# Kernel optimization log

Hardware: AMD Instinct MI355X
Metric: run time of the kernel (lower is better)

The kernel has to match this reference:

```python
import jax, jax.numpy as jnp
import numpy as np

N_NODES = 50000
N_EDGES = 600000
D_IN = 128
D_OUT = 128
N_BASES = 4
N_RATINGS = 5


def setup_inputs() -> dict:
    key = jax.random.key(0)
    k1, k2, k3, k4, k5, k6 = jax.random.split(key, 6)
    x = jax.random.normal(k1, (N_NODES, D_IN), dtype=jnp.float32)
    edge_index = jax.random.randint(k2, (2, N_EDGES), 0, N_NODES, dtype=jnp.int64)
    edge_type = jax.random.randint(k3, (N_EDGES,), 0, N_RATINGS, dtype=jnp.int64)
    # basis matrices B_k: (out, in); a_r stacked over ratings: (R, K); W_0: (out, in)
    B = jax.random.normal(k4, (N_BASES, D_OUT, D_IN), dtype=jnp.float32) * 0.05
    A = jax.random.normal(k5, (N_RATINGS, N_BASES), dtype=jnp.float32) * 0.05
    W0 = jax.random.normal(k6, (D_OUT, D_IN), dtype=jnp.float32) * 0.05
    return {"x": x, "edge_index": edge_index, "edge_type": edge_type, "B": B, "A": A, "W0": W0}


def reference(x, edge_index, edge_type, B, A, W0):
    # self-loop term: (W0 @ x^T)^T == x @ W0^T
    n_nodes = x.shape[0]
    src, tgt = edge_index[0], edge_index[1]
    out = x @ W0.T  # [N, out]
    # per-relation basis-composed weights W_r = sum_k a_r[k] * B_k  -> [R, out, in]
    W = jnp.einsum('rk,kod->rod', A, B)
    n_ratings = A.shape[0]
    for r in range(n_ratings):  # small fixed relation set
        h = x @ W[r].T                     # [N, out] transform once per node
        msg = jnp.where((edge_type == r)[:, None], h[src], jnp.float32(0))  # [E, out]
        out = out + jax.ops.segment_sum(msg, tgt, num_segments=n_nodes)
    return out
```

## Files before the change

kernel.cpp:

```cpp
#include <hip/hip_runtime.h>

#define N_NODES 50000
#define N_EDGES 600000
#define D 128
#define NB_SCAN 196

typedef __attribute__((ext_vector_type(8))) short short8;
typedef __attribute__((ext_vector_type(4))) float float4v;

static __device__ __forceinline__ float bf2f(unsigned int u16) {
    union { unsigned int i; float f; } v; v.i = u16 << 16; return v.f;
}
static __device__ __forceinline__ unsigned short f2bf(float f) {
    union { float f; unsigned int i; } v; v.f = f;
    unsigned int u = v.i;
    return (unsigned short)((u + 0x7FFFu + ((u >> 16) & 1u)) >> 16);
}
static __device__ __forceinline__ float h2f(unsigned int h) {
    unsigned int s = (h >> 15) & 1u, e = (h >> 10) & 0x1fu, m = h & 0x3ffu;
    unsigned int bits = (e == 0) ? (s << 31)
                                 : ((s << 31) | ((e + 112u) << 23) | (m << 13));
    union { unsigned int i; float f; } v; v.i = bits; return v.f;
}

__global__ __launch_bounds__(256) void setup(int* __restrict__ flags,
                                             int* __restrict__ cnt,
                                             unsigned int* __restrict__ scanst) {
    int i = blockIdx.x * 256 + threadIdx.x;
    if (i < N_NODES) cnt[i] = 0;
    if (i < 8) flags[i] = 0;
    if (i < 200) scanst[i] = 0;
}

__global__ __launch_bounds__(256) void detect_all(const int* __restrict__ ei,
                                                  const int* __restrict__ et,
                                                  const unsigned int* __restrict__ x,
                                                  const unsigned int* __restrict__ B,
                                                  const unsigned int* __restrict__ A,
                                                  const unsigned int* __restrict__ W0,
                                                  int* __restrict__ flags) {
    __shared__ int sflag;
    if (threadIdx.x == 0) sflag = 0;
    __syncthreads();
    int b = blockIdx.x, acc = 0, fidx;
    if (b < 192) {
        fidx = 0;
        for (int i = b * 256 + threadIdx.x; i < N_EDGES; i += 192 * 256)
            acc |= ei[2 * i + 1];
    } else if (b < 240) {
        fidx = 1;
        for (int i = (b - 192) * 256 + threadIdx.x; i < N_EDGES / 2; i += 48 * 256)
            acc |= et[2 * i + 1];
    } else if (b < 288) {
        fidx = 2;
        for (int i = (b - 240) * 256 + threadIdx.x; i < 600000; i += 48 * 256) {
            unsigned int e = (x[i] >> 7) & 0xffu;
            acc |= (e > 0xA0u || e < 0x50u) ? 1 : 0;
        }
    } else if (b < 300) {
        fidx = 3;
        for (int i = (b - 288) * 256 + threadIdx.x; i < 32768; i += 12 * 256) {
            unsigned int e = (B[i] >> 7) & 0xffu;
            acc |= (e > 0xA0u || e < 0x50u) ? 1 : 0;
        }
    } else if (b == 300) {
        fidx = 4;
        for (int i = threadIdx.x; i < 10; i += 256) {
            unsigned int e = (A[i] >> 7) & 0xffu;
            acc |= (e > 0xA0u || e < 0x50u) ? 1 : 0;
        }
    } else if (b < 307) {
        fidx = 5;
        for (int i = (b - 301) * 256 + threadIdx.x; i < 8192; i += 6 * 256) {
            unsigned int e = (W0[i] >> 7) & 0xffu;
            acc |= (e > 0xA0u || e < 0x50u) ? 1 : 0;
        }
    } else {
        fidx = 6;
        for (int i = (b - 307) * 256 + threadIdx.x; i < 300000; i += 48 * 256) {
            unsigned int el = (x[i] >> 7) & 0xffu, eh = (x[i] >> 23) & 0xffu;
            acc |= (el < 0x58u || eh < 0x58u) ? 1 : 0;
        }
    }
    if (acc) sflag = 1;
    __syncthreads();
    if (threadIdx.x == 0 && sflag) atomicOr(flags + fidx, 1);
}

static __device__ __forceinline__ float loadw(const void* p, int idx, int f32) {
    return f32 ? ((const float*)p)[idx] : bf2f(((const unsigned short*)p)[idx]);
}

__global__ __launch_bounds__(256) void norm_hist_w(const int* __restrict__ ei,
                                                   const int* __restrict__ et,
                                                   int* __restrict__ idx32,
                                                   int* __restrict__ et32,
                                                   int* __restrict__ cnt,
                                                   const void* __restrict__ A,
                                                   const void* __restrict__ B,
                                                   const void* __restrict__ W0,
                                                   unsigned short* __restrict__ wcatW,
                                                   const int* __restrict__ flags) {
    int b = blockIdx.x;
    if (b < 4688) {
        int i = b * 256 + threadIdx.x;
        if (i < 2 * N_EDGES) {
            int v = flags[0] ? ei[i] : ei[2 * i];
            idx32[i] = v;
            if (i >= N_EDGES && (unsigned)v < (unsigned)N_NODES)
                atomicAdd(&cnt[v], 1);
        }
    } else if (b < 7032) {
        int i = (b - 4688) * 256 + threadIdx.x;
        if (i < N_EDGES) et32[i] = flags[1] ? et[i] : et[2 * i];
    } else {
        int idx = (b - 7032) * 256 + threadIdx.x;
        int fB = flags[3], fA = flags[4], fW = flags[5];
        int f = idx >> 7, d = idx & 127;
        int slot = f >> 7, o = f & 127;
        float v;
        if (slot == 0) {
            v = loadw(W0, o * D + d, fW);
        } else {
            int r = slot - 1;
            v = 0.f;
#pragma unroll
            for (int j = 0; j < 4; ++j)
                v += loadw(A, r * 4 + j, fA) * loadw(B, (j * D + o) * D + d, fB);
        }
        wcatW[idx] = f2bf(v);
    }
}

__global__ __launch_bounds__(256) void prep_wt6_direct(const void* __restrict__ A,
                                                       const void* __restrict__ B,
                                                       const void* __restrict__ W0,
                                                       float* __restrict__ wcatT6F,
                                                       const int* __restrict__ flags) {
    int idx = blockIdx.x * 256 + threadIdx.x;
    int fB = flags[3], fA = flags[4], fW = flags[5];
    int slot = idx >> 14, d = (idx >> 7) & 127, o = idx & 127;
    float v;
    if (slot == 0) {
        v = loadw(W0, o * D + d, fW);
    } else {
        int r = slot - 1;
        v = 0.f;
#pragma unroll
        for (int j = 0; j < 4; ++j)
            v += loadw(A, r * 4 + j, fA) * loadw(B, (j * D + o) * D + d, fB);
    }
    wcatT6F[idx] = v;
}

__global__ __launch_bounds__(256) void gemm_y(const void* __restrict__ xraw,
                                              const unsigned short* __restrict__ wcatW,
                                              unsigned short* __restrict__ Ybf,
                                              const int* __restrict__ flags) {
    __shared__ unsigned short xs[64 * 136];
    __shared__ unsigned short wsd[128 * 136];
    int tid = threadIdx.x;
    int m0 = blockIdx.x * 64;
    int wid = tid >> 6, lane = tid & 63;
    int wm = (wid & 1) * 32, wn = (wid >> 1) * 64;
    int lm = lane & 15, kg = lane >> 4;
    int f32 = flags[2], f16 = flags[6];
    const short8 z8 = {0, 0, 0, 0, 0, 0, 0, 0};

    {
        int row = tid >> 2, cseg = (tid & 3) * 32;
        int gm = m0 + row;
        short8 av[4];
        if (gm >= N_NODES) {
#pragma unroll
            for (int q = 0; q < 4; ++q) av[q] = z8;
        } else if (f32) {
            const float4* xp = (const float4*)xraw + (((size_t)gm * D + cseg) >> 2);
#pragma unroll
            for (int q = 0; q < 4; ++q) {
                float4 u0 = xp[2 * q], u1 = xp[2 * q + 1];
                union { short8 s; unsigned short h[8]; } pk;
                pk.h[0] = f2bf(u0.x); pk.h[1] = f2bf(u0.y);
                pk.h[2] = f2bf(u0.z); pk.h[3] = f2bf(u0.w);
                pk.h[4] = f2bf(u1.x); pk.h[5] = f2bf(u1.y);
                pk.h[6] = f2bf(u1.z); pk.h[7] = f2bf(u1.w);
                av[q] = pk.s;
            }
        } else if (f16) {
            const uint4* xp4 = (const uint4*)xraw + (((size_t)gm * D + cseg) >> 3);
#pragma unroll
            for (int q = 0; q < 4; ++q) {
                uint4 u = xp4[q];
                unsigned int ww[4] = {u.x, u.y, u.z, u.w};
                union { short8 s; unsigned short h[8]; } pk;
#pragma unroll
                for (int z = 0; z < 4; ++z) {
                    pk.h[2 * z]     = f2bf(h2f(ww[z] & 0xffffu));
                    pk.h[2 * z + 1] = f2bf(h2f(ww[z] >> 16));
                }
                av[q] = pk.s;
            }
        } else {
            const uint4* xp4 = (const uint4*)xraw + (((size_t)gm * D + cseg) >> 3);
#pragma unroll
            for (int q = 0; q < 4; ++q) {
                union { uint4 v; short8 s; } cv; cv.v = xp4[q];
                av[q] = cv.s;
            }
        }
#pragma unroll
        for (int q = 0; q < 4; ++q)
            *(short8*)(&xs[row * 136 + cseg + q * 8]) = av[q];
    }

    for (int nt = 0; nt < 6; ++nt) {
        if (nt) __syncthreads();
        {
            int row = tid >> 1, cseg = (tid & 1) * 64;
            const unsigned short* wp = wcatW + (size_t)(nt * 128 + row) * D + cseg;
#pragma unroll
            for (int q = 0; q < 8; ++q)
                *(short8*)(&wsd[row * 136 + cseg + q * 8]) = *(const short8*)(wp + q * 8);
        }
        __syncthreads();

        float4v accf[2][4];
#pragma unroll
        for (int i = 0; i < 2; ++i)
#pragma unroll
            for (int j = 0; j < 4; ++j) accf[i][j] = (float4v){0.f, 0.f, 0.f, 0.f};

#pragma unroll
        for (int kb = 0; kb < 4; ++kb) {
            int k = kb * 32 + kg * 8;
            short8 a[2], b[4];
#pragma unroll
            for (int i = 0; i < 2; ++i)
                a[i] = *(const short8*)(&xs[(wm + i * 16 + lm) * 136 + k]);
#pragma unroll
            for (int j = 0; j < 4; ++j)
                b[j] = *(const short8*)(&wsd[(wn + j * 16 + lm) * 136 + k]);
#pragma unroll
            for (int i = 0; i < 2; ++i)
#pragma unroll
                for (int j = 0; j < 4; ++j)
                    accf[i][j] = __builtin_amdgcn_mfma_f32_16x16x32_bf16(a[i], b[j], accf[i][j], 0, 0, 0);
        }

#pragma unroll
        for (int i = 0; i < 2; ++i) {
            int gmb = m0 + wm + i * 16 + kg * 4;
#pragma unroll
            for (int j = 0; j < 4; ++j) {
                int gn = nt * 128 + wn + j * 16 + lm;
#pragma unroll
                for (int r = 0; r < 4; ++r) {
                    int gm = gmb + r;
                    if (gm < N_NODES) Ybf[(size_t)gm * 768 + gn] = f2bf(accf[i][j][r]);
                }
            }
        }
    }
}

#define SC_AGG (1u << 30)
#define SC_PRE (1u << 31)
__global__ __launch_bounds__(256) void scan_place(const int* __restrict__ cnt,
                                                  int* __restrict__ offsets,
                                                  int* __restrict__ cursor,
                                                  unsigned int* __restrict__ scanst,
                                                  const int* __restrict__ src,
                                                  const int* __restrict__ tgt,
                                                  const int* __restrict__ et,
                                                  int* __restrict__ entries) {
    __shared__ int sh[256];
    __shared__ int sbid, sprefix;
    unsigned int* status = scanst;
    unsigned int* ticket = scanst + 196;
    unsigned int* done   = scanst + 197;
    int t = threadIdx.x;
    if (t == 0) sbid = (int)atomicAdd(ticket, 1u);
    __syncthreads();
    int bid = sbid;
    int idx = bid * 256 + t;
    int v = (idx < N_NODES) ? cnt[idx] : 0;
    sh[t] = v;
    __syncthreads();
    for (int off = 1; off < 256; off <<= 1) {
        int a = (t >= off) ? sh[t - off] : 0;
        __syncthreads();
        sh[t] += a;
        __syncthreads();
    }
    if (t == 0) {
        int total = sh[255];
        atomicExch(&status[bid], (unsigned int)total | SC_AGG);
        int prefix = 0;
        for (int j = bid - 1; j >= 0; --j) {
            unsigned int s;
            do { s = atomicAdd(&status[j], 0u); } while ((s & (SC_AGG | SC_PRE)) == 0u);
            prefix += (int)(s & 0x3FFFFFFFu);
            if (s & SC_PRE) break;
        }
        atomicExch(&status[bid], (unsigned int)(prefix + total) | SC_PRE);
        sprefix = prefix;
    }
    __syncthreads();
    int excl = sh[t] - v + sprefix;
    if (idx < N_NODES) {
        offsets[idx] = excl;
        atomicExch(&cursor[idx], excl);
        if (idx == N_NODES - 1) offsets[N_NODES] = excl + v;
    }
    __syncthreads();
    if (t == 0) {
        atomicAdd(done, 1u);
        while (atomicAdd(done, 0u) < (unsigned)NB_SCAN) __builtin_amdgcn_s_sleep(1);
    }
    __syncthreads();
    int e0 = bid * 3062;
    int e1 = e0 + 3062; if (e1 > N_EDGES) e1 = N_EDGES;
    for (int e = e0 + t; e < e1; e += 256) {
        int s = src[e], g = tgt[e], r = et[e];
        if ((unsigned)s >= (unsigned)N_NODES || (unsigned)g >= (unsigned)N_NODES || (unsigned)r >= 5u) continue;
        int pos = atomicAdd(&cursor[g], 1);
        entries[pos] = s * 8 + r;
    }
}

__global__ __launch_bounds__(256) void agg_out(const int* __restrict__ offsets,
                                               const int* __restrict__ entries,
                                               const unsigned int* __restrict__ Y32,
                                               float* __restrict__ outF) {
    int tid = threadIdx.x;
    int wid = tid >> 6, lane = tid & 63;
    int n = __builtin_amdgcn_readfirstlane(blockIdx.x * 4 + wid);
    int beg = __builtin_amdgcn_readfirstlane(offsets[n]);
    int end = __builtin_amdgcn_readfirstlane(offsets[n + 1]);
    unsigned int selfw = Y32[(size_t)n * 384 + lane];
    float a0 = bf2f(selfw & 0xffffu), a1 = bf2f(selfw >> 16);

    for (int base = beg; base < end; base += 64) {
        int cnt = end - base;
        if (cnt > 64) cnt = 64;
        int eload = entries[base + lane];
        int j = 0;
        for (; j + 3 < cnt; j += 4) {
            int en0 = __builtin_amdgcn_readlane(eload, j);
            int en1 = __builtin_amdgcn_readlane(eload, j + 1);
            int en2 = __builtin_amdgcn_readlane(eload, j + 2);
            int en3 = __builtin_amdgcn_readlane(eload, j + 3);
            unsigned int r0 = (unsigned)(en0 >> 3) < (unsigned)N_NODES ? (unsigned)(en0 >> 3) : 0u;
            unsigned int r1 = (unsigned)(en1 >> 3) < (unsigned)N_NODES ? (unsigned)(en1 >> 3) : 0u;
            unsigned int r2 = (unsigned)(en2 >> 3) < (unsigned)N_NODES ? (unsigned)(en2 >> 3) : 0u;
            unsigned int r3 = (unsigned)(en3 >> 3) < (unsigned)N_NODES ? (unsigned)(en3 >> 3) : 0u;
            unsigned int x0 = Y32[(size_t)r0 * 384 + ((en0 & 7) + 1) * 64 + lane];
            unsigned int x1 = Y32[(size_t)r1 * 384 + ((en1 & 7) + 1) * 64 + lane];
            unsigned int x2 = Y32[(size_t)r2 * 384 + ((en2 & 7) + 1) * 64 + lane];
            unsigned int x3 = Y32[(size_t)r3 * 384 + ((en3 & 7) + 1) * 64 + lane];
            a0 += bf2f(x0 & 0xffffu); a1 += bf2f(x0 >> 16);
            a0 += bf2f(x1 & 0xffffu); a1 += bf2f(x1 >> 16);
            a0 += bf2f(x2 & 0xffffu); a1 += bf2f(x2 >> 16);
            a0 += bf2f(x3 & 0xffffu); a1 += bf2f(x3 >> 16);
        }
        for (; j < cnt; ++j) {
            int en = __builtin_amdgcn_readlane(eload, j);
            unsigned int rr = (unsigned)(en >> 3) < (unsigned)N_NODES ? (unsigned)(en >> 3) : 0u;
            unsigned int xw = Y32[(size_t)rr * 384 + ((en & 7) + 1) * 64 + lane];
            a0 += bf2f(xw & 0xffffu); a1 += bf2f(xw >> 16);
        }
    }

    *((float2*)outF + (size_t)n * 64 + lane) = make_float2(a0, a1);
}

static __device__ __forceinline__ float2 readx2(const void* x, int node, int lane,
                                                int f32, int f16) {
    if (f32) return *((const float2*)x + (size_t)node * 64 + lane);
    unsigned int w = *((const unsigned int*)x + (size_t)node * 64 + lane);
    float2 r;
    if (f16) { r.x = h2f(w & 0xffffu); r.y = h2f(w >> 16); }
    else     { r.x = bf2f(w & 0xffffu); r.y = bf2f(w >> 16); }
    return r;
}

__global__ __launch_bounds__(256) void self_raw(const void* __restrict__ x,
                                                const float* __restrict__ wcatT6F,
                                                float* __restrict__ outF,
                                                const int* __restrict__ flags) {
    int t = blockIdx.x * 256 + threadIdx.x;
    int n = t >> 6, lane = t & 63;
    int f32 = flags[2], f16 = flags[6];
    float2 xp = readx2(x, n, lane, f32, f16);
    float m0 = 0.f, m1 = 0.f;
#pragma unroll 8
    for (int dp = 0; dp < 64; ++dp) {
        float xa = __shfl(xp.x, dp);
        float xc = __shfl(xp.y, dp);
        float2 w0 = *(const float2*)(wcatT6F + (size_t)(2 * dp) * D + 2 * lane);
        float2 w1 = *(const float2*)(wcatT6F + (size_t)(2 * dp + 1) * D + 2 * lane);
        m0 += xa * w0.x + xc * w1.x;
        m1 += xa * w0.y + xc * w1.y;
    }
    *((float2*)outF + (size_t)n * 64 + lane) = make_float2(m0, m1);
}

__global__ __launch_bounds__(256) void edge_raw(const int* __restrict__ src,
                                                const int* __restrict__ tgt,
                                                const int* __restrict__ et,
                                                const void* __restrict__ x,
                                                const float* __restrict__ wcatT6F,
                                                float* __restrict__ outF,
                                                const int* __restrict__ flags) {
    int t = blockIdx.x * 256 + threadIdx.x;
    int e = t >> 6, lane = t & 63;
    if (e >= N_EDGES) return;
    int f32 = flags[2], f16 = flags[6];
    int s = src[e], g = tgt[e], r = et[e];
    if ((unsigned)s >= (unsigned)N_NODES || (unsigned)g >= (unsigned)N_NODES || (unsigned)r >= 5u) return;
    float2 xp = readx2(x, s, lane, f32, f16);
    const float* wt = wcatT6F + (size_t)(1 + r) * D * D;
    float m0 = 0.f, m1 = 0.f;
#pragma unroll 8
    for (int dp = 0; dp < 64; ++dp) {
        float xa = __shfl(xp.x, dp);
        float xc = __shfl(xp.y, dp);
        float2 w0 = *(const float2*)(wt + (size_t)(2 * dp) * D + 2 * lane);
        float2 w1 = *(const float2*)(wt + (size_t)(2 * dp + 1) * D + 2 * lane);
        m0 += xa * w0.x + xc * w1.x;
        m1 += xa * w0.y + xc * w1.y;
    }
    float* ap = outF + (size_t)g * D + lane * 2;
    atomicAdd(ap + 0, m0);
    atomicAdd(ap + 1, m1);
}

extern "C" void kernel_launch(void* const* d_in, const int* in_sizes, int n_in,
                              void* d_out, int out_size, void* d_ws, size_t ws_size,
                              hipStream_t stream) {
    const void* x  = nullptr; const int* ei = nullptr; const int* et = nullptr;
    const void* B  = nullptr; const void* A = nullptr; const void* W0 = nullptr;
    for (int i = 0; i < n_in; ++i) {
        switch (in_sizes[i]) {
            case 6400000: x  = d_in[i]; break;
            case 1200000: ei = (const int*)d_in[i]; break;
            case 600000:  et = (const int*)d_in[i]; break;
            case 65536:   B  = d_in[i]; break;
            case 20:      A  = d_in[i]; break;
            case 16384:   W0 = d_in[i]; break;
            default: break;
        }
    }
    if (!x || !ei || !et || !B || !A || !W0) {
        x  = d_in[0]; ei = (const int*)d_in[1]; et = (const int*)d_in[2];
        B  = d_in[3]; A  = d_in[4]; W0 = d_in[5];
    }
    float* outF = (float*)d_out;

    char* ws = (char*)d_ws;
    int*   flags   = (int*)(ws + 0);
    float* wcatT6F = (float*)(ws + 256);
    unsigned short* wcatW = (unsigned short*)(ws + 393472);
    int* offsets  = (int*)(ws + 590080);
    int* cursor   = (int*)(ws + 790144);
    int* cnt      = (int*)(ws + 990144);
    unsigned int* scanst = (unsigned int*)(ws + 1190144);
    int* entries  = (int*)(ws + 1191168);
    int* idx32    = (int*)(ws + 3591168);
    int* et32     = (int*)(ws + 8391168);
    unsigned short* Y = (unsigned short*)(ws + 10791168);
    const size_t needMain = 10791168ull + 76800000ull;
    const size_t needT3   = 393472ull;

    int* src32 = idx32;
    int* tgt32 = idx32 + N_EDGES;

    setup<<<NB_SCAN, 256, 0, stream>>>(flags, cnt, scanst);
    detect_all<<<355, 256, 0, stream>>>(ei, et, (const unsigned int*)x,
                                        (const unsigned int*)B, (const unsigned int*)A,
                                        (const unsigned int*)W0, flags);

    if (ws_size >= needMain) {
        norm_hist_w<<<7416, 256, 0, stream>>>(ei, et, idx32, et32, cnt,
                                              A, B, W0, wcatW, flags);
        gemm_y<<<782, 256, 0, stream>>>(x, wcatW, Y, flags);
        scan_place<<<NB_SCAN, 256, 0, stream>>>(cnt, offsets, cursor, scanst,
                                                src32, tgt32, et32, entries);
        agg_out<<<12500, 256, 0, stream>>>(offsets, entries, (const unsigned int*)Y, outF);
    } else if (ws_size >= needT3) {
        prep_wt6_direct<<<384, 256, 0, stream>>>(A, B, W0, wcatT6F, flags);
        self_raw<<<12500, 256, 0, stream>>>(x, wcatT6F, outF, flags);
        edge_raw<<<150000, 256, 0, stream>>>(ei, ei + N_EDGES, et, x, wcatT6F, outF, flags);
    }
}
```

Measured before the change: 242.0 us.

## Swizzle LDS, swap MFMA operands for packed stores, prefetch next weight tile

The gemm_y kernel now uses XOR-swizzled LDS layouts in place of padded rows. It swaps the MFMA operand roles, with weights as A and nodes as B, so each lane holds four consecutive output features and can write them as one 8-byte store instead of four scattered 2-byte stores. It also prefetches the next 128-row weight tile into registers while the current tile is computed, which hides global load latency. The cost is more register use from the prefetch buffer and more complex indexing.

```diff
diff --git a/kernel.cpp b/kernel.cpp
--- a/kernel.cpp
+++ b/kernel.cpp
@@ -153,44 +153,44 @@
     wcatT6F[idx] = v;
 }
 
+#define SWZ(row, cb) ((row) * 256 + ((cb) ^ (((row) & 7) << 4)))
 __global__ __launch_bounds__(256) void gemm_y(const void* __restrict__ xraw,
                                               const unsigned short* __restrict__ wcatW,
                                               unsigned short* __restrict__ Ybf,
                                               const int* __restrict__ flags) {
-    __shared__ unsigned short xs[64 * 136];
-    __shared__ unsigned short wsd[128 * 136];
+    __shared__ __align__(16) char lds[49152];
+    char* xsb = lds;
+    char* wsb = lds + 16384;
     int tid = threadIdx.x;
     int m0 = blockIdx.x * 64;
     int wid = tid >> 6, lane = tid & 63;
-    int wm = (wid & 1) * 32, wn = (wid >> 1) * 64;
+    int wf = (wid & 1) * 64;
+    int wn2 = (wid >> 1) * 32;
     int lm = lane & 15, kg = lane >> 4;
     int f32 = flags[2], f16 = flags[6];
     const short8 z8 = {0, 0, 0, 0, 0, 0, 0, 0};
 
     {
-        int row = tid >> 2, cseg = (tid & 3) * 32;
+        int row = tid >> 2, cb0 = (tid & 3) * 64;
         int gm = m0 + row;
-        short8 av[4];
-        if (gm >= N_NODES) {
-#pragma unroll
-            for (int q = 0; q < 4; ++q) av[q] = z8;
-        } else if (f32) {
-            const float4* xp = (const float4*)xraw + (((size_t)gm * D + cseg) >> 2);
-#pragma unroll
-            for (int q = 0; q < 4; ++q) {
-                float4 u0 = xp[2 * q], u1 = xp[2 * q + 1];
+#pragma unroll
+        for (int q = 0; q < 4; ++q) {
+            int cb = cb0 + q * 16;
+            short8 av;
+            if (gm >= N_NODES) {
+                av = z8;
+            } else if (f32) {
+                const float4* xp = (const float4*)xraw + (((size_t)gm * D) >> 2) + (cb >> 4) * 2;
+                float4 u0 = xp[0], u1 = xp[1];
                 union { short8 s; unsigned short h[8]; } pk;
                 pk.h[0] = f2bf(u0.x); pk.h[1] = f2bf(u0.y);
                 pk.h[2] = f2bf(u0.z); pk.h[3] = f2bf(u0.w);
                 pk.h[4] = f2bf(u1.x); pk.h[5] = f2bf(u1.y);
                 pk.h[6] = f2bf(u1.z); pk.h[7] = f2bf(u1.w);
-                av[q] = pk.s;
-            }
-        } else if (f16) {
-            const uint4* xp4 = (const uint4*)xraw + (((size_t)gm * D + cseg) >> 3);
-#pragma unroll
-            for (int q = 0; q < 4; ++q) {
-                uint4 u = xp4[q];
+                av = pk.s;
+            } else if (f16) {
+                const uint4* xp4 = (const uint4*)xraw + (((size_t)gm * D) >> 3) + (cb >> 4);
+                uint4 u = *xp4;
                 unsigned int ww[4] = {u.x, u.y, u.z, u.w};
                 union { short8 s; unsigned short h[8]; } pk;
 #pragma unroll
@@ -198,65 +198,74 @@
                     pk.h[2 * z]     = f2bf(h2f(ww[z] & 0xffffu));
                     pk.h[2 * z + 1] = f2bf(h2f(ww[z] >> 16));
                 }
-                av[q] = pk.s;
+                av = pk.s;
+            } else {
+                const uint4* xp4 = (const uint4*)xraw + (((size_t)gm * D) >> 3) + (cb >> 4);
+                union { uint4 v; short8 s; } cv; cv.v = *xp4;
+                av = cv.s;
             }
-        } else {
-            const uint4* xp4 = (const uint4*)xraw + (((size_t)gm * D + cseg) >> 3);
-#pragma unroll
-            for (int q = 0; q < 4; ++q) {
-                union { uint4 v; short8 s; } cv; cv.v = xp4[q];
-                av[q] = cv.s;
-            }
-        }
-#pragma unroll
-        for (int q = 0; q < 4; ++q)
-            *(short8*)(&xs[row * 136 + cseg + q * 8]) = av[q];
+            *(short8*)(xsb + SWZ(row, cb)) = av;
+        }
+    }
+
+    short8 wr[8];
+    {
+        int row = tid >> 1, c0h = (tid & 1) * 64;
+        const unsigned short* wp = wcatW + (size_t)row * D + c0h;
+#pragma unroll
+        for (int q = 0; q < 8; ++q) wr[q] = *(const short8*)(wp + q * 8);
     }
 
     for (int nt = 0; nt < 6; ++nt) {
         if (nt) __syncthreads();
         {
-            int row = tid >> 1, cseg = (tid & 1) * 64;
-            const unsigned short* wp = wcatW + (size_t)(nt * 128 + row) * D + cseg;
+            int row = tid >> 1, cb0 = (tid & 1) * 128;
 #pragma unroll
             for (int q = 0; q < 8; ++q)
-                *(short8*)(&wsd[row * 136 + cseg + q * 8]) = *(const short8*)(wp + q * 8);
+                *(short8*)(wsb + SWZ(row, cb0 + q * 16)) = wr[q];
+        }
+        if (nt + 1 < 6) {
+            int row = tid >> 1, c0h = (tid & 1) * 64;
+            const unsigned short* wp = wcatW + (size_t)((nt + 1) * 128 + row) * D + c0h;
+#pragma unroll
+            for (int q = 0; q < 8; ++q) wr[q] = *(const short8*)(wp + q * 8);
         }
         __syncthreads();
 
-        float4v accf[2][4];
-#pragma unroll
-        for (int i = 0; i < 2; ++i)
-#pragma unroll
-            for (int j = 0; j < 4; ++j) accf[i][j] = (float4v){0.f, 0.f, 0.f, 0.f};
+        float4v accf[4][2];
+#pragma unroll
+        for (int i = 0; i < 4; ++i)
+#pragma unroll
+            for (int j = 0; j < 2; ++j) accf[i][j] = (float4v){0.f, 0.f, 0.f, 0.f};
 
 #pragma unroll
         for (int kb = 0; kb < 4; ++kb) {
-            int k = kb * 32 + kg * 8;
-            short8 a[2], b[4];
-#pragma unroll
-            for (int i = 0; i < 2; ++i)
-                a[i] = *(const short8*)(&xs[(wm + i * 16 + lm) * 136 + k]);
-#pragma unroll
-            for (int j = 0; j < 4; ++j)
-                b[j] = *(const short8*)(&wsd[(wn + j * 16 + lm) * 136 + k]);
-#pragma unroll
-            for (int i = 0; i < 2; ++i)
-#pragma unroll
-                for (int j = 0; j < 4; ++j)
+            int kcb = kb * 64 + kg * 16;
+            short8 a[4], b[2];
+#pragma unroll
+            for (int i = 0; i < 4; ++i)
+                a[i] = *(const short8*)(wsb + SWZ(wf + i * 16 + lm, kcb));
+#pragma unroll
+            for (int j = 0; j < 2; ++j)
+                b[j] = *(const short8*)(xsb + SWZ(wn2 + j * 16 + lm, kcb));
+#pragma unroll
+            for (int i = 0; i < 4; ++i)
+#pragma unroll
+                for (int j = 0; j < 2; ++j)
                     accf[i][j] = __builtin_amdgcn_mfma_f32_16x16x32_bf16(a[i], b[j], accf[i][j], 0, 0, 0);
         }
 
 #pragma unroll
-        for (int i = 0; i < 2; ++i) {
-            int gmb = m0 + wm + i * 16 + kg * 4;
-#pragma unroll
-            for (int j = 0; j < 4; ++j) {
-                int gn = nt * 128 + wn + j * 16 + lm;
-#pragma unroll
-                for (int r = 0; r < 4; ++r) {
-                    int gm = gmb + r;
-                    if (gm < N_NODES) Ybf[(size_t)gm * 768 + gn] = f2bf(accf[i][j][r]);
+        for (int i = 0; i < 4; ++i) {
+            int f0 = nt * 128 + wf + i * 16 + kg * 4;
+#pragma unroll
+            for (int j = 0; j < 2; ++j) {
+                int node = m0 + wn2 + j * 16 + lm;
+                if (node < N_NODES) {
+                    union { unsigned long long u; unsigned short h[4]; } pk;
+                    pk.h[0] = f2bf(accf[i][j][0]); pk.h[1] = f2bf(accf[i][j][1]);
+                    pk.h[2] = f2bf(accf[i][j][2]); pk.h[3] = f2bf(accf[i][j][3]);
+                    *(unsigned long long*)(Ybf + (size_t)node * 768 + f0) = pk.u;
                 }
             }
         }
```

Result: no change. 245.0 us (+1.2%).
